# Performance work log

Measured on AMD Instinct MI355X. Metric: run time of the kernel, lower is better.

The kernel has to match this reference:

```python
import jax, jax.numpy as jnp
import numpy as np

T, B, D, H, L = 512, 128, 256, 256, 4


def setup_inputs() -> dict:
    key = jax.random.key(0)
    ks = jax.random.split(key, 12)
    s = 0.05  # weight scale for stable gating
    lengths = jnp.sort(jax.random.randint(ks[1], (B,), 1, T + 1))[::-1].astype(jnp.int32)
    return {
        "x": jax.random.normal(ks[0], (T, B, D), jnp.float32),
        "lengths": lengths,  # sorted descending, as in a PackedSequence
        "Wr": jax.random.normal(ks[2], (D + H, H), jnp.float32) * s,
        "Wz": jax.random.normal(ks[3], (D + H, H), jnp.float32) * s,
        "Wl": jax.random.normal(ks[4], (D + H, H), jnp.float32) * s,
        "Wt": jax.random.normal(ks[5], (D, H), jnp.float32) * s,
        "Cx": jax.random.normal(ks[6], (D, H), jnp.float32) * s,
        "Ch": jax.random.normal(ks[7], (H, H), jnp.float32) * s,
        "Tr": jax.random.normal(ks[8], (L, H, H), jnp.float32) * s,
        "Tz": jax.random.normal(ks[9], (L, H, H), jnp.float32) * s,
        "Tn": jax.random.normal(ks[10], (L, H, H), jnp.float32) * s,
    }


def _cell(xt, h, Wr, Wz, Wl, Wt, Cx, Ch, Tr, Tz, Tn):
    # LinearEnchancedGRU
    cat = jnp.concatenate([xt, h], axis=-1)  # [B, D+H]
    r = jax.nn.sigmoid(cat @ Wr)
    z = jax.nn.sigmoid(cat @ Wz)
    l = jax.nn.sigmoid(cat @ Wl)
    n = jnp.tanh(xt @ Cx + r * (h @ Ch)) + l * (xt @ Wt)
    h = (1.0 - z) * h + z * n
    # stack of TransitionGRU cells (fixed small depth)
    for i in range(Tr.shape[0]):
        rr = jax.nn.sigmoid(h @ Tr[i])
        zz = jax.nn.sigmoid(h @ Tz[i])
        nn_ = jnp.tanh(rr * (h @ Tn[i]))
        h = (1.0 - zz) * nn_ + zz * h
    return h


def reference(x, lengths, Wr, Wz, Wl, Wt, Cx, Ch, Tr, Tz, Tn):
    # Packed-sequence semantics: at step t only the first batchSizes[t] rows are
    # active (lengths sorted descending => mask[t] = t < lengths). Inactive rows
    # keep their old hidden (equivalent to hx[:batch] truncation) and emit 0
    # (row absent from the packed output).
    Tn_steps, Bn, _ = x.shape
    Hn = Ch.shape[0]
    mask = jnp.arange(Tn_steps)[:, None] < lengths[None, :]  # [T, B]

    def step(h, inp):
        xt, m = inp
        hn = _cell(xt, h, Wr, Wz, Wl, Wt, Cx, Ch, Tr, Tz, Tn)
        m = m[:, None]
        h = jnp.where(m, hn, h)
        out = jnp.where(m, hn, jnp.zeros_like(hn))
        return h, out

    h0 = jnp.zeros((Bn, Hn), x.dtype)
    _, outs = jax.lax.scan(step, h0, (x, mask))
    return outs  # [T, B, H], zero-padded beyond each sequence's length
```

## Files before the change

### kernel.cpp

```cpp
#include <hip/hip_runtime.h>
#include <hip/hip_bf16.h>
#include <string.h>

#define T_STEPS 512
#define BATCH   128
#define DIM     256
#define HID     256
#define NLAYERS 4

typedef unsigned int  uint4v  __attribute__((ext_vector_type(4)));
typedef unsigned int  uint2v  __attribute__((ext_vector_type(2)));
typedef short         short8  __attribute__((ext_vector_type(8)));
typedef float         float4v __attribute__((ext_vector_type(4)));

#define SLOT_BYTES  (128 * 1024)
#define NSLOTS      4
#define HBUF_BYTES  (NSLOTS * SLOT_BYTES)

__device__ __forceinline__ short8 as_s8(uint4v u) {
  union { uint4v u; short8 s; } x; x.u = u; return x.s;
}
__device__ __forceinline__ float sigf(float x) {
  return 1.0f / (1.0f + __expf(-x));
}
__device__ __forceinline__ float tanh_fast(float x) {
  x = fminf(fmaxf(x, -15.0f), 15.0f);
  float e = __expf(2.0f * x);
  return (e - 1.0f) / (e + 1.0f);
}
__device__ __forceinline__ unsigned short f2bf(float a) {
  unsigned ua = __builtin_bit_cast(unsigned, a);
  return (unsigned short)((ua + 0x7FFFu + ((ua >> 16) & 1u)) >> 16);
}
__device__ __forceinline__ unsigned pack_bf16x2(float a, float b) {
  return (unsigned)f2bf(a) | ((unsigned)f2bf(b) << 16);
}
__device__ __forceinline__ uint4v extract_frag(uint4v a, uint4v b) {
  uint4v f; f.x = a.x; f.y = a.z; f.z = b.x; f.w = b.z; return f;
}
__device__ __forceinline__ unsigned tagbad(uint4v a, uint4v b, unsigned tag) {
  return (a.y ^ tag) | (a.w ^ tag) | (b.y ^ tag) | (b.w ^ tag);
}

#define GLD16(A0,B0,A1,B1,A2,B2,A3,B3,A4,B4,A5,B5,A6,B6,A7,B7, ADDR)       \
  asm volatile(                                                             \
      "global_load_dwordx4 %0, %16, off offset:0 sc0 sc1\n\t"               \
      "global_load_dwordx4 %1, %16, off offset:16 sc0 sc1\n\t"              \
      "global_load_dwordx4 %2, %16, off offset:128 sc0 sc1\n\t"             \
      "global_load_dwordx4 %3, %16, off offset:144 sc0 sc1\n\t"             \
      "global_load_dwordx4 %4, %16, off offset:256 sc0 sc1\n\t"             \
      "global_load_dwordx4 %5, %16, off offset:272 sc0 sc1\n\t"             \
      "global_load_dwordx4 %6, %16, off offset:384 sc0 sc1\n\t"             \
      "global_load_dwordx4 %7, %16, off offset:400 sc0 sc1\n\t"             \
      "global_load_dwordx4 %8, %16, off offset:512 sc0 sc1\n\t"             \
      "global_load_dwordx4 %9, %16, off offset:528 sc0 sc1\n\t"             \
      "global_load_dwordx4 %10, %16, off offset:640 sc0 sc1\n\t"            \
      "global_load_dwordx4 %11, %16, off offset:656 sc0 sc1\n\t"            \
      "global_load_dwordx4 %12, %16, off offset:768 sc0 sc1\n\t"            \
      "global_load_dwordx4 %13, %16, off offset:784 sc0 sc1\n\t"            \
      "global_load_dwordx4 %14, %16, off offset:896 sc0 sc1\n\t"            \
      "global_load_dwordx4 %15, %16, off offset:912 sc0 sc1\n\t"            \
      "s_waitcnt vmcnt(0)"                                                  \
      : "=&v"(A0), "=&v"(B0), "=&v"(A1), "=&v"(B1),                         \
        "=&v"(A2), "=&v"(B2), "=&v"(A3), "=&v"(B3),                         \
        "=&v"(A4), "=&v"(B4), "=&v"(A5), "=&v"(B5),                         \
        "=&v"(A6), "=&v"(B6), "=&v"(A7), "=&v"(B7)                          \
      : "v"(ADDR)                                                           \
      : "memory")

#define POLL8T(F0,F1,F2,F3,F4,F5,F6,F7, ADDR, TAG)                          \
  {                                                                         \
    uint4v _a0,_b0,_a1,_b1,_a2,_b2,_a3,_b3,_a4,_b4,_a5,_b5,_a6,_b6,_a7,_b7; \
    for (int _it = 0;; ++_it) {                                             \
      GLD16(_a0,_b0,_a1,_b1,_a2,_b2,_a3,_b3,_a4,_b4,_a5,_b5,_a6,_b6,_a7,_b7,\
            ADDR);                                                          \
      unsigned _bad = tagbad(_a0,_b0,TAG) | tagbad(_a1,_b1,TAG) |           \
                      tagbad(_a2,_b2,TAG) | tagbad(_a3,_b3,TAG) |           \
                      tagbad(_a4,_b4,TAG) | tagbad(_a5,_b5,TAG) |           \
                      tagbad(_a6,_b6,TAG) | tagbad(_a7,_b7,TAG);            \
      if (__all((int)(_bad == 0u)) || _it > (1 << 16)) break;               \
      if (_it >= 16) __builtin_amdgcn_s_sleep(1);                           \
    }                                                                       \
    F0 = extract_frag(_a0,_b0); F1 = extract_frag(_a1,_b1);                 \
    F2 = extract_frag(_a2,_b2); F3 = extract_frag(_a3,_b3);                 \
    F4 = extract_frag(_a4,_b4); F5 = extract_frag(_a5,_b5);                 \
    F6 = extract_frag(_a6,_b6); F7 = extract_frag(_a7,_b7);                 \
  }

#define PUBLISH(ADDR, PACKED, TAG)                                          \
  {                                                                         \
    uint2v _pv; _pv.x = (PACKED); _pv.y = (TAG);                            \
    asm volatile("global_store_dwordx2 %0, %1, off sc0 sc1"                 \
                 :: "v"(ADDR), "v"(_pv) : "memory");                        \
  }

#define MFMA_K8(ACC, BARR, H0,H1,H2,H3,H4,H5,H6,H7)                                  \
  ACC = __builtin_amdgcn_mfma_f32_16x16x32_bf16(as_s8(H0), BARR[0], ACC, 0, 0, 0);   \
  ACC = __builtin_amdgcn_mfma_f32_16x16x32_bf16(as_s8(H1), BARR[1], ACC, 0, 0, 0);   \
  ACC = __builtin_amdgcn_mfma_f32_16x16x32_bf16(as_s8(H2), BARR[2], ACC, 0, 0, 0);   \
  ACC = __builtin_amdgcn_mfma_f32_16x16x32_bf16(as_s8(H3), BARR[3], ACC, 0, 0, 0);   \
  ACC = __builtin_amdgcn_mfma_f32_16x16x32_bf16(as_s8(H4), BARR[4], ACC, 0, 0, 0);   \
  ACC = __builtin_amdgcn_mfma_f32_16x16x32_bf16(as_s8(H5), BARR[5], ACC, 0, 0, 0);   \
  ACC = __builtin_amdgcn_mfma_f32_16x16x32_bf16(as_s8(H6), BARR[6], ACC, 0, 0, 0);   \
  ACC = __builtin_amdgcn_mfma_f32_16x16x32_bf16(as_s8(H7), BARR[7], ACC, 0, 0, 0);

__launch_bounds__(256, 1)
__global__ void rnn_main(const float* __restrict__ x,
                         const int* __restrict__ lengths,
                         const float* __restrict__ Wr,
                         const float* __restrict__ Wz,
                         const float* __restrict__ Wl,
                         const float* __restrict__ Wt,
                         const float* __restrict__ Cx,
                         const float* __restrict__ Ch,
                         const float* __restrict__ Tr,
                         const float* __restrict__ Tz,
                         const float* __restrict__ Tn,
                         unsigned char* __restrict__ hbuf,
                         float* __restrict__ out) {
  const int tid  = threadIdx.x;
  const int lane = tid & 63;
  const int v    = tid >> 6;
  const int bid  = blockIdx.x;
  const int c    = bid & 7;
  const int w    = bid >> 3;

  __shared__ float  tiles[6][16 * 20];
  __shared__ uint4v hsh[8][64];
  __shared__ int    len_sh[16];

  short8 Wf[6][8];
  {
    const int SCHED[4][6] = {{0, 4, 9, 10, 11, 12},
                             {1, 5, 13, 14, 15, 16},
                             {2, 6, 17, 18, 19, 20},
                             {3, 7, 8, 3, 3, 3}};
    const int colg = w * 16 + (lane & 15);
#pragma unroll
    for (int s = 0; s < 6; ++s) {
      const int m = SCHED[v][s];
      const float* base;
      int ro = 0;
      if      (m == 0)  { base = Wr; ro = 256; }
      else if (m == 1)  { base = Wz; ro = 256; }
      else if (m == 2)  { base = Wl; ro = 256; }
      else if (m == 3)  { base = Ch; }
      else if (m == 4)  { base = Wr; }
      else if (m == 5)  { base = Wz; }
      else if (m == 6)  { base = Wl; }
      else if (m == 7)  { base = Cx; }
      else if (m == 8)  { base = Wt; }
      else if (m <= 12) { base = Tr + (size_t)(m - 9)  * HID * HID; }
      else if (m <= 16) { base = Tz + (size_t)(m - 13) * HID * HID; }
      else              { base = Tn + (size_t)(m - 17) * HID * HID; }
#pragma unroll
      for (int kt = 0; kt < 8; ++kt) {
        const int k0 = ro + kt * 32 + (lane >> 4) * 8;
        short8 f;
#pragma unroll
        for (int j = 0; j < 8; ++j)
          f[j] = (short)f2bf(base[(size_t)(k0 + j) * HID + colg]);
        Wf[s][kt] = f;
      }
    }
  }

  if (tid < 16) len_sh[tid] = lengths[c * 16 + tid];
  __syncthreads();

  const int row = tid >> 4;
  const int col = tid & 15;
  const int mylen = len_sh[row];
  const int ci = col * 20 + row;

  float hreg = 0.0f, hprev = 0.0f;

  const unsigned vh = (unsigned)((c * 16 + (lane & 15)) * 1024 + (lane >> 4) * 32);
  const unsigned pub_off =
      (unsigned)(((c * 16 + (tid >> 4)) * 128 + w * 8 + ((tid & 15) >> 1)) * 8);
  const float* xbase =
      x + ((size_t)c * 16 + (lane & 15)) * DIM + (lane >> 4) * 8;

  for (int t = 0; t < T_STEPS; ++t) {
    const int r0 = t * 5;
    {
      const float* xp = xbase + (size_t)t * BATCH * DIM;
      uint4v xf[8];
#pragma unroll
      for (int kt = 0; kt < 8; ++kt) {
        float4v xa = *(const float4v*)(xp + kt * 32);
        float4v xb = *(const float4v*)(xp + kt * 32 + 4);
        uint4v f;
        f.x = pack_bf16x2(xa.x, xa.y);
        f.y = pack_bf16x2(xa.z, xa.w);
        f.z = pack_bf16x2(xb.x, xb.y);
        f.w = pack_bf16x2(xb.z, xb.w);
        xf[kt] = f;
      }

      float4v a0 = {0.f, 0.f, 0.f, 0.f};
      float4v a1 = {0.f, 0.f, 0.f, 0.f};
      float4v a2 = {0.f, 0.f, 0.f, 0.f};
      if (v < 3) {
#pragma unroll
        for (int kt = 0; kt < 8; ++kt)
          a0 = __builtin_amdgcn_mfma_f32_16x16x32_bf16(as_s8(xf[kt]), Wf[1][kt], a0, 0, 0, 0);
      } else {
#pragma unroll
        for (int kt = 0; kt < 8; ++kt)
          a1 = __builtin_amdgcn_mfma_f32_16x16x32_bf16(as_s8(xf[kt]), Wf[1][kt], a1, 0, 0, 0);
#pragma unroll
        for (int kt = 0; kt < 8; ++kt)
          a2 = __builtin_amdgcn_mfma_f32_16x16x32_bf16(as_s8(xf[kt]), Wf[2][kt], a2, 0, 0, 0);
      }
      uint4v h0, h1, h2, h3, h4, h5, h6, h7;
      if (v == 0) {
        const unsigned char* ap =
            hbuf + (size_t)((r0 - 1) & 3) * SLOT_BYTES + vh;
        POLL8T(h0, h1, h2, h3, h4, h5, h6, h7, ap, (unsigned)r0);
        hsh[0][lane] = h0; hsh[1][lane] = h1; hsh[2][lane] = h2;
        hsh[3][lane] = h3; hsh[4][lane] = h4; hsh[5][lane] = h5;
        hsh[6][lane] = h6; hsh[7][lane] = h7;
      }
      __syncthreads();
      if (v != 0) {
        h0 = hsh[0][lane]; h1 = hsh[1][lane]; h2 = hsh[2][lane];
        h3 = hsh[3][lane]; h4 = hsh[4][lane]; h5 = hsh[5][lane];
        h6 = hsh[6][lane]; h7 = hsh[7][lane];
      }
      MFMA_K8(a0, Wf[0], h0, h1, h2, h3, h4, h5, h6, h7);
      {
        float* tp = &tiles[(v < 3) ? v : 3][(lane & 15) * 20 + (lane >> 4) * 4];
        *(float4v*)tp = a0;
        if (v == 3) {
          *(float4v*)&tiles[4][(lane & 15) * 20 + (lane >> 4) * 4] = a1;
          *(float4v*)&tiles[5][(lane & 15) * 20 + (lane >> 4) * 4] = a2;
        }
      }
      __syncthreads();
      float rp  = tiles[0][ci], zp = tiles[1][ci], lp = tiles[2][ci];
      float chv = tiles[3][ci], xcv = tiles[4][ci], xwv = tiles[5][ci];
      float r  = sigf(rp), z = sigf(zp), lg = sigf(lp);
      float n  = tanh_fast(xcv + r * chv) + lg * xwv;
      hreg = (1.0f - z) * hreg + z * n;
      {
        float hp = __shfl_xor(hreg, 1);
        if (!(tid & 1)) {
          unsigned char* pp = hbuf + (size_t)(r0 & 3) * SLOT_BYTES + pub_off;
          PUBLISH(pp, pack_bf16x2(hreg, hp), (unsigned)(r0 + 1));
        }
      }
    }
#pragma unroll
    for (int i = 0; i < NLAYERS; ++i) {
      const int ri = r0 + 1 + i;
      uint4v h0, h1, h2, h3, h4, h5, h6, h7;
      if (v == 0) {
        const unsigned char* ap =
            hbuf + (size_t)((ri - 1) & 3) * SLOT_BYTES + vh;
        POLL8T(h0, h1, h2, h3, h4, h5, h6, h7, ap, (unsigned)ri);
        hsh[0][lane] = h0; hsh[1][lane] = h1; hsh[2][lane] = h2;
        hsh[3][lane] = h3; hsh[4][lane] = h4; hsh[5][lane] = h5;
        hsh[6][lane] = h6; hsh[7][lane] = h7;
      }
      __syncthreads();
      if (v < 3) {
        if (v != 0) {
          h0 = hsh[0][lane]; h1 = hsh[1][lane]; h2 = hsh[2][lane];
          h3 = hsh[3][lane]; h4 = hsh[4][lane]; h5 = hsh[5][lane];
          h6 = hsh[6][lane]; h7 = hsh[7][lane];
        }
        float4v a = {0.f, 0.f, 0.f, 0.f};
        MFMA_K8(a, Wf[2 + i], h0, h1, h2, h3, h4, h5, h6, h7);
        *(float4v*)&tiles[v][(lane & 15) * 20 + (lane >> 4) * 4] = a;
      }
      __syncthreads();
      float rr = sigf(tiles[0][ci]);
      float zz = sigf(tiles[1][ci]);
      float nn = tanh_fast(rr * tiles[2][ci]);
      hreg = (1.0f - zz) * nn + zz * hreg;
      if (i == NLAYERS - 1) {
        const bool act = (t < mylen);
        float hv = act ? hreg : hprev;
        float ov = act ? hreg : 0.0f;
        hreg = hv;
        hprev = hv;
        out[((size_t)t * BATCH + c * 16 + row) * HID + w * 16 + col] = ov;
      }
      {
        float hp = __shfl_xor(hreg, 1);
        if (!(tid & 1)) {
          unsigned char* pp = hbuf + (size_t)(ri & 3) * SLOT_BYTES + pub_off;
          PUBLISH(pp, pack_bf16x2(hreg, hp), (unsigned)(ri + 1));
        }
      }
    }
  }
}

extern "C" void kernel_launch(void* const* d_in, const int* in_sizes, int n_in,
                              void* d_out, int out_size, void* d_ws, size_t ws_size,
                              hipStream_t stream) {
  (void)in_sizes; (void)n_in; (void)out_size; (void)ws_size;
  const float* x        = (const float*)d_in[0];
  const int* lengths    = (const int*)d_in[1];
  const float* Wr       = (const float*)d_in[2];
  const float* Wz       = (const float*)d_in[3];
  const float* Wl       = (const float*)d_in[4];
  const float* Wt       = (const float*)d_in[5];
  const float* Cx       = (const float*)d_in[6];
  const float* Ch       = (const float*)d_in[7];
  const float* Tr       = (const float*)d_in[8];
  const float* Tz       = (const float*)d_in[9];
  const float* Tn       = (const float*)d_in[10];

  unsigned char* hbuf = (unsigned char*)d_ws;

  hipMemsetAsync(hbuf, 0x00, HBUF_BYTES, stream);

  rnn_main<<<dim3(128), dim3(256), 0, stream>>>(
      x, lengths, Wr, Wz, Wl, Wt, Cx, Ch, Tr, Tz, Tn,
      hbuf, (float*)d_out);
}
```

Measured before the change: 9.177 ms.

## Prefetch next-step x into LDS, split MFMA accumulators, drain stores on non-polling waves

Wave 1 loads the next timestep's x during the transition layers, converts it to bf16 and stages it in shared memory, so x loads leave the critical path at the start of each step. The serial 8-deep MFMA accumulation chains are split into two interleaved accumulators to shorten the dependency latency on the recurrent path. Non-polling waves now wait for their outstanding publish stores to finish, which may speed cross-block visibility but adds stalls. The design relies on the existing barriers to keep the xsh write and read ordered, and it adds register pressure from holding the prefetched x.

```diff
diff --git a/kernel.cpp b/kernel.cpp
--- a/kernel.cpp
+++ b/kernel.cpp
@@ -94,15 +94,18 @@
                  :: "v"(ADDR), "v"(_pv) : "memory");                        \
   }
 
-#define MFMA_K8(ACC, BARR, H0,H1,H2,H3,H4,H5,H6,H7)                                  \
-  ACC = __builtin_amdgcn_mfma_f32_16x16x32_bf16(as_s8(H0), BARR[0], ACC, 0, 0, 0);   \
-  ACC = __builtin_amdgcn_mfma_f32_16x16x32_bf16(as_s8(H1), BARR[1], ACC, 0, 0, 0);   \
-  ACC = __builtin_amdgcn_mfma_f32_16x16x32_bf16(as_s8(H2), BARR[2], ACC, 0, 0, 0);   \
-  ACC = __builtin_amdgcn_mfma_f32_16x16x32_bf16(as_s8(H3), BARR[3], ACC, 0, 0, 0);   \
-  ACC = __builtin_amdgcn_mfma_f32_16x16x32_bf16(as_s8(H4), BARR[4], ACC, 0, 0, 0);   \
-  ACC = __builtin_amdgcn_mfma_f32_16x16x32_bf16(as_s8(H5), BARR[5], ACC, 0, 0, 0);   \
-  ACC = __builtin_amdgcn_mfma_f32_16x16x32_bf16(as_s8(H6), BARR[6], ACC, 0, 0, 0);   \
-  ACC = __builtin_amdgcn_mfma_f32_16x16x32_bf16(as_s8(H7), BARR[7], ACC, 0, 0, 0);
+#define DRAIN_STORES                                                        \
+  { asm volatile("s_waitcnt vmcnt(0)" ::: "memory"); }
+
+#define MFMA_K8_2(AX, AY, BARR, H0,H1,H2,H3,H4,H5,H6,H7)                             \
+  AX = __builtin_amdgcn_mfma_f32_16x16x32_bf16(as_s8(H0), BARR[0], AX, 0, 0, 0);     \
+  AY = __builtin_amdgcn_mfma_f32_16x16x32_bf16(as_s8(H1), BARR[1], AY, 0, 0, 0);     \
+  AX = __builtin_amdgcn_mfma_f32_16x16x32_bf16(as_s8(H2), BARR[2], AX, 0, 0, 0);     \
+  AY = __builtin_amdgcn_mfma_f32_16x16x32_bf16(as_s8(H3), BARR[3], AY, 0, 0, 0);     \
+  AX = __builtin_amdgcn_mfma_f32_16x16x32_bf16(as_s8(H4), BARR[4], AX, 0, 0, 0);     \
+  AY = __builtin_amdgcn_mfma_f32_16x16x32_bf16(as_s8(H5), BARR[5], AY, 0, 0, 0);     \
+  AX = __builtin_amdgcn_mfma_f32_16x16x32_bf16(as_s8(H6), BARR[6], AX, 0, 0, 0);     \
+  AY = __builtin_amdgcn_mfma_f32_16x16x32_bf16(as_s8(H7), BARR[7], AY, 0, 0, 0);
 
 __launch_bounds__(256, 1)
 __global__ void rnn_main(const float* __restrict__ x,
@@ -127,6 +130,7 @@
 
   __shared__ float  tiles[6][16 * 20];
   __shared__ uint4v hsh[8][64];
+  __shared__ uint4v xsh[8][64];
   __shared__ int    len_sh[16];
 
   short8 Wf[6][8];
@@ -166,6 +170,23 @@
   }
 
   if (tid < 16) len_sh[tid] = lengths[c * 16 + tid];
+
+  const float* xbase =
+      x + ((size_t)c * 16 + (lane & 15)) * DIM + (lane >> 4) * 8;
+
+  if (v == 1) {
+#pragma unroll
+    for (int kt = 0; kt < 8; ++kt) {
+      float4v xa = *(const float4v*)(xbase + kt * 32);
+      float4v xb = *(const float4v*)(xbase + kt * 32 + 4);
+      uint4v f;
+      f.x = pack_bf16x2(xa.x, xa.y);
+      f.y = pack_bf16x2(xa.z, xa.w);
+      f.z = pack_bf16x2(xb.x, xb.y);
+      f.w = pack_bf16x2(xb.z, xb.w);
+      xsh[kt][lane] = f;
+    }
+  }
   __syncthreads();
 
   const int row = tid >> 4;
@@ -178,25 +199,14 @@
   const unsigned vh = (unsigned)((c * 16 + (lane & 15)) * 1024 + (lane >> 4) * 32);
   const unsigned pub_off =
       (unsigned)(((c * 16 + (tid >> 4)) * 128 + w * 8 + ((tid & 15) >> 1)) * 8);
-  const float* xbase =
-      x + ((size_t)c * 16 + (lane & 15)) * DIM + (lane >> 4) * 8;
 
   for (int t = 0; t < T_STEPS; ++t) {
     const int r0 = t * 5;
+    float4v xra[8], xrb[8];
     {
-      const float* xp = xbase + (size_t)t * BATCH * DIM;
       uint4v xf[8];
 #pragma unroll
-      for (int kt = 0; kt < 8; ++kt) {
-        float4v xa = *(const float4v*)(xp + kt * 32);
-        float4v xb = *(const float4v*)(xp + kt * 32 + 4);
-        uint4v f;
-        f.x = pack_bf16x2(xa.x, xa.y);
-        f.y = pack_bf16x2(xa.z, xa.w);
-        f.z = pack_bf16x2(xb.x, xb.y);
-        f.w = pack_bf16x2(xb.z, xb.w);
-        xf[kt] = f;
-      }
+      for (int kt = 0; kt < 8; ++kt) xf[kt] = xsh[kt][lane];
 
       float4v a0 = {0.f, 0.f, 0.f, 0.f};
       float4v a1 = {0.f, 0.f, 0.f, 0.f};
@@ -228,7 +238,12 @@
         h3 = hsh[3][lane]; h4 = hsh[4][lane]; h5 = hsh[5][lane];
         h6 = hsh[6][lane]; h7 = hsh[7][lane];
       }
-      MFMA_K8(a0, Wf[0], h0, h1, h2, h3, h4, h5, h6, h7);
+      {
+        float4v ahx = {0.f, 0.f, 0.f, 0.f};
+        float4v ahy = {0.f, 0.f, 0.f, 0.f};
+        MFMA_K8_2(ahx, ahy, Wf[0], h0, h1, h2, h3, h4, h5, h6, h7);
+        a0 = a0 + ahx + ahy;
+      }
       {
         float* tp = &tiles[(v < 3) ? v : 3][(lane & 15) * 20 + (lane >> 4) * 4];
         *(float4v*)tp = a0;
@@ -249,11 +264,33 @@
           unsigned char* pp = hbuf + (size_t)(r0 & 3) * SLOT_BYTES + pub_off;
           PUBLISH(pp, pack_bf16x2(hreg, hp), (unsigned)(r0 + 1));
         }
+        if (v != 0) DRAIN_STORES;
       }
     }
 #pragma unroll
     for (int i = 0; i < NLAYERS; ++i) {
       const int ri = r0 + 1 + i;
+      if (v == 1 && t + 1 < T_STEPS) {
+        if (i == 0) {
+          const float* xq = xbase + (size_t)(t + 1) * BATCH * DIM;
+#pragma unroll
+          for (int kt = 0; kt < 8; ++kt) {
+            xra[kt] = *(const float4v*)(xq + kt * 32);
+            xrb[kt] = *(const float4v*)(xq + kt * 32 + 4);
+          }
+        }
+        if (i == 1) {
+#pragma unroll
+          for (int kt = 0; kt < 8; ++kt) {
+            uint4v f;
+            f.x = pack_bf16x2(xra[kt].x, xra[kt].y);
+            f.y = pack_bf16x2(xra[kt].z, xra[kt].w);
+            f.z = pack_bf16x2(xrb[kt].x, xrb[kt].y);
+            f.w = pack_bf16x2(xrb[kt].z, xrb[kt].w);
+            xsh[kt][lane] = f;
+          }
+        }
+      }
       uint4v h0, h1, h2, h3, h4, h5, h6, h7;
       if (v == 0) {
         const unsigned char* ap =
@@ -270,9 +307,11 @@
           h3 = hsh[3][lane]; h4 = hsh[4][lane]; h5 = hsh[5][lane];
           h6 = hsh[6][lane]; h7 = hsh[7][lane];
         }
-        float4v a = {0.f, 0.f, 0.f, 0.f};
-        MFMA_K8(a, Wf[2 + i], h0, h1, h2, h3, h4, h5, h6, h7);
-        *(float4v*)&tiles[v][(lane & 15) * 20 + (lane >> 4) * 4] = a;
+        float4v ahx = {0.f, 0.f, 0.f, 0.f};
+        float4v ahy = {0.f, 0.f, 0.f, 0.f};
+        MFMA_K8_2(ahx, ahy, Wf[2 + i], h0, h1, h2, h3, h4, h5, h6, h7);
+        ahx = ahx + ahy;
+        *(float4v*)&tiles[v][(lane & 15) * 20 + (lane >> 4) * 4] = ahx;
       }
       __syncthreads();
       float rr = sigf(tiles[0][ci]);
@@ -293,6 +332,7 @@
           unsigned char* pp = hbuf + (size_t)(ri & 3) * SLOT_BYTES + pub_off;
           PUBLISH(pp, pack_bf16x2(hreg, hp), (unsigned)(ri + 1));
         }
+        if (v != 0) DRAIN_STORES;
       }
     }
   }
```

Result: faster. 7.571 ms (-17.5%).
